# Optimization experiments

Measured on AMD Instinct MI355X. Metric: run time of the kernel, lower is better.

Reference implementation:

```python
import jax, jax.numpy as jnp
import numpy as np

EPS_F = 1e-6  # epsilon used when normalizing F^T F (as in EIGNN/MGNNI)


def _g(F):
    # g(F) = F^T F / (||F^T F||_F + eps): symmetric PSD, spectral radius <= 1
    FF = F.T @ F
    return FF / (jnp.linalg.norm(FF) + EPS_F)


def setup_inputs() -> dict:
    m, n = 128, 8192
    key = jax.random.key(0)
    k1, k2, k3, k4 = jax.random.split(key, 4)
    X = jax.random.normal(k1, (m, n), dtype=jnp.float32)
    # learned mixing matrix, init 1/sqrt(m) * randn as in __init__
    F = (1.0 / np.sqrt(m)) * jax.random.normal(k2, (m, m), dtype=jnp.float32)
    # precomputed eigendecomposition of the (normalized) adjacency S:
    # eigenvector matrix Q_S (n,n) and eigenvalues Lambda_S stored as (n,1)
    Q_S = jax.random.normal(k3, (n, n), dtype=jnp.float32) / np.sqrt(n)
    Lambda_S = (0.99 * (2.0 * jax.random.uniform(k4, (n, 1), dtype=jnp.float32) - 1.0))
    gamma = jnp.float32(0.8)
    return {"X": X, "F": F, "Q_S": Q_S, "Lambda_S": Lambda_S, "gamma": gamma}


def reference(X, F, Q_S, Lambda_S, gamma):
    # IDMFunction.forward: closed-form solve of Z = gamma * g(F) Z S + X
    # via eigendecompositions g(F) = Q_F diag(Lam_F) Q_F^T, S = Q_S diag(Lam_S) Q_S^T
    Lam_F, Q_F = jnp.linalg.eigh(_g(F))                         # (m,), (m,m)
    # G[i,j] = 1 / (1 - gamma * Lam_F[i] * Lam_S[j])            # (m,n)
    G = 1.0 / (1.0 - gamma * Lam_F[:, None] * Lambda_S.reshape(1, -1))
    # Z = Q_F (G * (Q_F^T X Q_S)) Q_S^T                          # (m,n)
    Z = Q_F @ (G * (Q_F.T @ X @ Q_S)) @ Q_S.T
    return Z
```

## Files before the change

### kernel.cpp

```cpp
#include <hip/hip_runtime.h>
#include <math.h>

#define EPS_F 1e-6f

typedef __attribute__((ext_vector_type(8))) short short8;
typedef __attribute__((ext_vector_type(4))) float f32x4;
typedef unsigned long long ull;

static __device__ __forceinline__ unsigned short f2bf(float f) {
    unsigned u = __float_as_uint(f);
    u += 0x7fff + ((u >> 16) & 1);
    return (unsigned short)(u >> 16);
}
static __device__ __forceinline__ ull pack4(float a, float b, float c, float d) {
    return (ull)f2bf(a) | ((ull)f2bf(b) << 16) | ((ull)f2bf(c) << 32) | ((ull)f2bf(d) << 48);
}
static __device__ __forceinline__ float bf2f(unsigned short s) {
    return __uint_as_float(((unsigned)s) << 16);
}


__global__ void kff(const float* __restrict__ F, float* __restrict__ FF) {
    int i = blockIdx.x, j = threadIdx.x;
    float s = 0.f;
    for (int k = 0; k < 128; ++k) s += F[k*128 + i] * F[k*128 + j];
    FF[i*128 + j] = s;
}

__global__ void knorm(const float* __restrict__ FF, float* __restrict__ inv) {
    float s = 0.f;
    for (int idx = threadIdx.x; idx < 128*128; idx += 256) { float v = FF[idx]; s += v*v; }
    for (int o = 32; o > 0; o >>= 1) s += __shfl_down(s, o);
    __shared__ float wsum[4];
    int lane = threadIdx.x & 63, w = threadIdx.x >> 6;
    if (lane == 0) wsum[w] = s;
    __syncthreads();
    if (threadIdx.x == 0) inv[0] = 1.f / (sqrtf(wsum[0]+wsum[1]+wsum[2]+wsum[3]) + EPS_F);
}

__global__ void kxbf(const float* __restrict__ X, short* __restrict__ Xb) {
    int i = blockIdx.x*blockDim.x + threadIdx.x;
    const float4* p = (const float4*)(X + (size_t)i*8);
    float4 v0 = p[0], v1 = p[1];
    *(ull*)&Xb[(size_t)i*8    ] = pack4(v0.x, v0.y, v0.z, v0.w);
    *(ull*)&Xb[(size_t)i*8 + 4] = pack4(v1.x, v1.y, v1.z, v1.w);
}

template<bool TRANSB>
__global__ __launch_bounds__(256) void gemm_p3(
    const short* __restrict__ Ab, const float* __restrict__ Qg,
    float* __restrict__ Cp, int N, int K, int KC)
{
    constexpr int LDT = 40;
    constexpr int ASZ = 128 * LDT;
    constexpr int BSZ = 64 * LDT;
    __shared__ short As[3 * ASZ];
    __shared__ short Bs[3 * BSZ];

    const int t    = threadIdx.x;
    const int lane = t & 63;
    const int w    = t >> 6;
    const int wm   = (w >> 1) * 64;
    const int wn   = (w & 1)  * 32;
    const int l16  = lane & 15;
    const int lq   = lane >> 4;
    const int n0   = blockIdx.x * 64;
    const int kb   = blockIdx.y * KC;
    const int NS   = KC >> 5;

    float* Cout = Cp + (size_t)blockIdx.y * (128 * 8192);

    const int ar0 = t >> 2, ako = (t & 3) * 8;
    const int br0 = t >> 3, bko = (t & 7) * 4;
    const int bn  = t & 63, bkh = t >> 6;

    f32x4 acc[4][2];
    #pragma unroll
    for (int i = 0; i < 4; ++i) { acc[i][0] = (f32x4){0,0,0,0}; acc[i][1] = (f32x4){0,0,0,0}; }

    short8 saA0, saA1, saB0, saB1;
    float4 sbA0, sbA1, sbB0, sbB1;
    float  sbtA[8], sbtB[8];

#define LOAD_T(k0, SA0, SA1, SB0, SB1, SBT) do {                                  \
        SA0 = *(const short8*)&Ab[(size_t)ar0*K + (k0) + ako];                    \
        SA1 = *(const short8*)&Ab[(size_t)(ar0+64)*K + (k0) + ako];               \
        if constexpr (TRANSB) {                                                   \
            SB0 = *(const float4*)&Qg[(size_t)(n0+br0   )*K + (k0) + bko];        \
            SB1 = *(const float4*)&Qg[(size_t)(n0+br0+32)*K + (k0) + bko];        \
        } else {                                                                  \
            _Pragma("unroll")                                                     \
            for (int j = 0; j < 8; ++j)                                           \
                SBT[j] = Qg[(size_t)((k0) + bkh*8 + j)*N + n0 + bn];              \
        }                                                                         \
    } while (0)

#define WRITE_T(buf, SA0, SA1, SB0, SB1, SBT) do {                                \
        short* asb = &As[(buf)*ASZ];                                              \
        short* bsb = &Bs[(buf)*BSZ];                                              \
        *(short8*)&asb[ar0*LDT + ako]      = SA0;                                 \
        *(short8*)&asb[(ar0+64)*LDT + ako] = SA1;                                 \
        if constexpr (TRANSB) {                                                   \
            *(ull*)&bsb[br0*LDT + bko]      = pack4(SB0.x, SB0.y, SB0.z, SB0.w);  \
            *(ull*)&bsb[(br0+32)*LDT + bko] = pack4(SB1.x, SB1.y, SB1.z, SB1.w);  \
        } else {                                                                  \
            short8 p;                                                             \
            _Pragma("unroll")                                                     \
            for (int j = 0; j < 8; ++j) p[j] = (short)f2bf(SBT[j]);               \
            *(short8*)&bsb[bn*LDT + bkh*8] = p;                                   \
        }                                                                         \
    } while (0)

#define MFMA_T(buf) do {                                                          \
        const short* asb = &As[(buf)*ASZ];                                        \
        const short* bsb = &Bs[(buf)*BSZ];                                        \
        short8 af[4], bfr[2];                                                     \
        _Pragma("unroll")                                                         \
        for (int mt = 0; mt < 4; ++mt)                                            \
            af[mt] = *(const short8*)&asb[(wm + mt*16 + l16)*LDT + lq*8];         \
        bfr[0] = *(const short8*)&bsb[(wn      + l16)*LDT + lq*8];                \
        bfr[1] = *(const short8*)&bsb[(wn + 16 + l16)*LDT + lq*8];                \
        _Pragma("unroll")                                                         \
        for (int mt = 0; mt < 4; ++mt) {                                          \
            acc[mt][0] = __builtin_amdgcn_mfma_f32_16x16x32_bf16(af[mt], bfr[0], acc[mt][0], 0, 0, 0); \
            acc[mt][1] = __builtin_amdgcn_mfma_f32_16x16x32_bf16(af[mt], bfr[1], acc[mt][1], 0, 0, 0); \
        }                                                                         \
    } while (0)

    LOAD_T(kb,      saA0, saA1, sbA0, sbA1, sbtA);
    LOAD_T(kb + 32, saB0, saB1, sbB0, sbB1, sbtB);
    WRITE_T(0, saA0, saA1, sbA0, sbA1, sbtA);
    __syncthreads();

    int b0 = 0, b1 = 1, b2 = 2;
    for (int ks = 0; ks < NS; ks += 2) {
        if (ks + 2 < NS) LOAD_T(kb + (ks+2)*32, saA0, saA1, sbA0, sbA1, sbtA);
        MFMA_T(b0);
        if (ks + 1 < NS) WRITE_T(b1, saB0, saB1, sbB0, sbB1, sbtB);
        __syncthreads();

        if (ks + 3 < NS) LOAD_T(kb + (ks+3)*32, saB0, saB1, sbB0, sbB1, sbtB);
        MFMA_T(b1);
        if (ks + 2 < NS) WRITE_T(b2, saA0, saA1, sbA0, sbA1, sbtA);
        __syncthreads();

        int tb = b0; b0 = b2; b2 = b1; b1 = tb;
    }

#undef LOAD_T
#undef WRITE_T
#undef MFMA_T

    #pragma unroll
    for (int mt = 0; mt < 4; ++mt)
        #pragma unroll
        for (int nt = 0; nt < 2; ++nt)
            #pragma unroll
            for (int r = 0; r < 4; ++r)
                Cout[(size_t)(wm + mt*16 + lq*4 + r)*N + n0 + wn + nt*16 + l16] = acc[mt][nt][r];
}

__global__ __launch_bounds__(512) void horner_fused(
    const float* __restrict__ FF, const float* __restrict__ invn,
    const float* __restrict__ lam, const float* __restrict__ gam,
    const float* __restrict__ Yp, short* __restrict__ Rg, int N)
{
    constexpr int LDT = 136;
    constexpr int T = 14;
    constexpr int SPL = 16;
    __shared__ short Abf[128 * LDT];
    __shared__ short Rs[32 * LDT];

    const int t    = threadIdx.x;
    const int lane = t & 63;
    const int w    = t >> 6;
    const int wm   = (w >> 1) * 32;
    const int wn   = (w & 1) * 16;
    const int l16  = lane & 15;
    const int lq   = lane >> 4;
    const int j0   = blockIdx.x * 32;

    #pragma unroll
    for (int i = 0; i < 8; ++i) {
        int flat = t + i*512;
        int m = flat >> 5, k4 = flat & 31;
        float4 v = *(const float4*)&FF[m*128 + k4*4];
        *(ull*)&Abf[m*LDT + k4*4] = pack4(v.x, v.y, v.z, v.w);
    }
    {
        int j = t & 31, mg = t >> 5;
        float vv[8];
        #pragma unroll
        for (int r2 = 0; r2 < 8; ++r2) {
            size_t idx = (size_t)(mg*8 + r2)*N + j0 + j;
            float s = 0.f;
            #pragma unroll
            for (int sp = 0; sp < SPL; ++sp) s += Yp[(size_t)sp*(128*8192) + idx];
            vv[r2] = s;
        }
        *(ull*)&Rs[j*LDT + mg*8    ] = pack4(vv[0], vv[1], vv[2], vv[3]);
        *(ull*)&Rs[j*LDT + mg*8 + 4] = pack4(vv[4], vv[5], vv[6], vv[7]);
    }
    __syncthreads();

    const int col = j0 + wn + l16;
    float yreg[2][4];
    #pragma unroll
    for (int mt = 0; mt < 2; ++mt)
        #pragma unroll
        for (int r = 0; r < 4; ++r)
            yreg[mt][r] = bf2f((unsigned short)Rs[(wn + l16)*LDT + wm + mt*16 + lq*4 + r]);
    const float s = gam[0] * lam[col] * invn[0];

    for (int it = 0; it < T; ++it) {
        f32x4 racc[2];
        racc[0] = (f32x4){0,0,0,0};
        racc[1] = (f32x4){0,0,0,0};
        #pragma unroll
        for (int kq = 0; kq < 4; ++kq) {
            short8 b  = *(const short8*)&Rs[(wn + l16)*LDT + kq*32 + lq*8];
            short8 a0 = *(const short8*)&Abf[(wm      + l16)*LDT + kq*32 + lq*8];
            short8 a1 = *(const short8*)&Abf[(wm + 16 + l16)*LDT + kq*32 + lq*8];
            racc[0] = __builtin_amdgcn_mfma_f32_16x16x32_bf16(a0, b, racc[0], 0, 0, 0);
            racc[1] = __builtin_amdgcn_mfma_f32_16x16x32_bf16(a1, b, racc[1], 0, 0, 0);
        }
        __syncthreads();
        #pragma unroll
        for (int mt = 0; mt < 2; ++mt) {
            float r0 = yreg[mt][0] + s*racc[mt][0];
            float r1 = yreg[mt][1] + s*racc[mt][1];
            float r2 = yreg[mt][2] + s*racc[mt][2];
            float r3 = yreg[mt][3] + s*racc[mt][3];
            if (it < T-1) {
                *(ull*)&Rs[(wn + l16)*LDT + wm + mt*16 + lq*4] = pack4(r0, r1, r2, r3);
            } else {
                int row = wm + mt*16 + lq*4;
                Rg[(size_t)(row+0)*N + col] = (short)f2bf(r0);
                Rg[(size_t)(row+1)*N + col] = (short)f2bf(r1);
                Rg[(size_t)(row+2)*N + col] = (short)f2bf(r2);
                Rg[(size_t)(row+3)*N + col] = (short)f2bf(r3);
            }
        }
        if (it < T-1) __syncthreads();
    }
}

__global__ __launch_bounds__(256) void zred(const float* __restrict__ Zp,
                                            float* __restrict__ Z) {
    int i = (blockIdx.x*blockDim.x + threadIdx.x) * 4;
    f32x4 s = (f32x4){0,0,0,0};
    #pragma unroll
    for (int sp = 0; sp < 8; ++sp) {
        const float4 v = *(const float4*)&Zp[(size_t)sp*(128*8192) + i];
        s[0] += v.x; s[1] += v.y; s[2] += v.z; s[3] += v.w;
    }
    *(f32x4*)&Z[i] = s;
}


extern "C" void kernel_launch(void* const* d_in, const int* in_sizes, int n_in,
                              void* d_out, int out_size, void* d_ws, size_t ws_size,
                              hipStream_t stream) {
    const float* X   = (const float*)d_in[0];
    const float* F   = (const float*)d_in[1];
    const float* Q   = (const float*)d_in[2];
    const float* lam = (const float*)d_in[3];
    const float* gam = (const float*)d_in[4];
    float* Z = (float*)d_out;

    const int N = 8192, K = 8192;

    char* ws = (char*)d_ws;
    float* FF  = (float*)(ws);
    float* inv = (float*)(ws + 65536);
    short* Xb  = (short*)(ws + 131072);
    short* Rg  = (short*)(ws + 2228224);
    float* Yp  = (float*)(ws + 4325376);
    float* Zp  = (float*)(ws + 4325376 + 67108864);

    hipLaunchKernelGGL(kff,   dim3(128), dim3(128), 0, stream, F, FF);
    hipLaunchKernelGGL(knorm, dim3(1),   dim3(256), 0, stream, FF, inv);
    hipLaunchKernelGGL(kxbf,  dim3(512), dim3(256), 0, stream, X, Xb);

    hipLaunchKernelGGL((gemm_p3<false>), dim3(128, 16), dim3(256), 0, stream,
                       Xb, Q, Yp, N, K, 512);

    hipLaunchKernelGGL(horner_fused, dim3(256), dim3(512), 0, stream,
                       FF, inv, lam, gam, Yp, Rg, N);

    hipLaunchKernelGGL((gemm_p3<true>), dim3(128, 8), dim3(256), 0, stream,
                       Rg, Q, Zp, N, K, 1024);

    hipLaunchKernelGGL(zred, dim3(1024), dim3(256), 0, stream, Zp, Z);
}
```

Before: 219.1 us.

## Halve split-K for first GEMM and switch to double-buffered LDS with lighter barriers

The first GEMM's split-K factor drops from 16 to 8 (KC 512 to 1024), and horner_fused now reduces 8 partial slices instead of 16. This halves the fp32 partial-sum traffic that goes to and from the Yp workspace. Both GEMMs move from triple-buffered to double-buffered shared memory, and __syncthreads is replaced by a barrier that waits only on LDS counters, which cuts LDS use and may raise occupancy. The cost is fewer blocks in the first GEMM, so parallelism is lower, and there is less slack between global loads and their use.

```diff
diff --git a/kernel.cpp b/kernel.cpp
--- a/kernel.cpp
+++ b/kernel.cpp
@@ -18,6 +18,12 @@
 static __device__ __forceinline__ float bf2f(unsigned short s) {
     return __uint_as_float(((unsigned)s) << 16);
 }
+
+#define BAR() do {                                            \
+        asm volatile("s_waitcnt lgkmcnt(0)" ::: "memory");    \
+        __builtin_amdgcn_s_barrier();                         \
+        __builtin_amdgcn_sched_barrier(0);                    \
+    } while (0)
 
 
 __global__ void kff(const float* __restrict__ F, float* __restrict__ FF) {
@@ -47,15 +53,15 @@
 }
 
 template<bool TRANSB>
-__global__ __launch_bounds__(256) void gemm_p3(
+__global__ __launch_bounds__(256) void gemm_pipe(
     const short* __restrict__ Ab, const float* __restrict__ Qg,
     float* __restrict__ Cp, int N, int K, int KC)
 {
     constexpr int LDT = 40;
     constexpr int ASZ = 128 * LDT;
     constexpr int BSZ = 64 * LDT;
-    __shared__ short As[3 * ASZ];
-    __shared__ short Bs[3 * BSZ];
+    __shared__ short As[2][ASZ];
+    __shared__ short Bs[2][BSZ];
 
     const int t    = threadIdx.x;
     const int lane = t & 63;
@@ -96,30 +102,26 @@
     } while (0)
 
 #define WRITE_T(buf, SA0, SA1, SB0, SB1, SBT) do {                                \
-        short* asb = &As[(buf)*ASZ];                                              \
-        short* bsb = &Bs[(buf)*BSZ];                                              \
-        *(short8*)&asb[ar0*LDT + ako]      = SA0;                                 \
-        *(short8*)&asb[(ar0+64)*LDT + ako] = SA1;                                 \
+        *(short8*)&As[buf][ar0*LDT + ako]      = SA0;                             \
+        *(short8*)&As[buf][(ar0+64)*LDT + ako] = SA1;                             \
         if constexpr (TRANSB) {                                                   \
-            *(ull*)&bsb[br0*LDT + bko]      = pack4(SB0.x, SB0.y, SB0.z, SB0.w);  \
-            *(ull*)&bsb[(br0+32)*LDT + bko] = pack4(SB1.x, SB1.y, SB1.z, SB1.w);  \
+            *(ull*)&Bs[buf][br0*LDT + bko]      = pack4(SB0.x, SB0.y, SB0.z, SB0.w); \
+            *(ull*)&Bs[buf][(br0+32)*LDT + bko] = pack4(SB1.x, SB1.y, SB1.z, SB1.w); \
         } else {                                                                  \
             short8 p;                                                             \
             _Pragma("unroll")                                                     \
             for (int j = 0; j < 8; ++j) p[j] = (short)f2bf(SBT[j]);               \
-            *(short8*)&bsb[bn*LDT + bkh*8] = p;                                   \
+            *(short8*)&Bs[buf][bn*LDT + bkh*8] = p;                               \
         }                                                                         \
     } while (0)
 
 #define MFMA_T(buf) do {                                                          \
-        const short* asb = &As[(buf)*ASZ];                                        \
-        const short* bsb = &Bs[(buf)*BSZ];                                        \
         short8 af[4], bfr[2];                                                     \
         _Pragma("unroll")                                                         \
         for (int mt = 0; mt < 4; ++mt)                                            \
-            af[mt] = *(const short8*)&asb[(wm + mt*16 + l16)*LDT + lq*8];         \
-        bfr[0] = *(const short8*)&bsb[(wn      + l16)*LDT + lq*8];                \
-        bfr[1] = *(const short8*)&bsb[(wn + 16 + l16)*LDT + lq*8];                \
+            af[mt] = *(const short8*)&As[buf][(wm + mt*16 + l16)*LDT + lq*8];     \
+        bfr[0] = *(const short8*)&Bs[buf][(wn      + l16)*LDT + lq*8];            \
+        bfr[1] = *(const short8*)&Bs[buf][(wn + 16 + l16)*LDT + lq*8];            \
         _Pragma("unroll")                                                         \
         for (int mt = 0; mt < 4; ++mt) {                                          \
             acc[mt][0] = __builtin_amdgcn_mfma_f32_16x16x32_bf16(af[mt], bfr[0], acc[mt][0], 0, 0, 0); \
@@ -130,21 +132,18 @@
     LOAD_T(kb,      saA0, saA1, sbA0, sbA1, sbtA);
     LOAD_T(kb + 32, saB0, saB1, sbB0, sbB1, sbtB);
     WRITE_T(0, saA0, saA1, sbA0, sbA1, sbtA);
-    __syncthreads();
-
-    int b0 = 0, b1 = 1, b2 = 2;
+    BAR();
+
     for (int ks = 0; ks < NS; ks += 2) {
         if (ks + 2 < NS) LOAD_T(kb + (ks+2)*32, saA0, saA1, sbA0, sbA1, sbtA);
-        MFMA_T(b0);
-        if (ks + 1 < NS) WRITE_T(b1, saB0, saB1, sbB0, sbB1, sbtB);
-        __syncthreads();
+        MFMA_T(0);
+        if (ks + 1 < NS) WRITE_T(1, saB0, saB1, sbB0, sbB1, sbtB);
+        BAR();
 
         if (ks + 3 < NS) LOAD_T(kb + (ks+3)*32, saB0, saB1, sbB0, sbB1, sbtB);
-        MFMA_T(b1);
-        if (ks + 2 < NS) WRITE_T(b2, saA0, saA1, sbA0, sbA1, sbtA);
-        __syncthreads();
-
-        int tb = b0; b0 = b2; b2 = b1; b1 = tb;
+        MFMA_T(1);
+        if (ks + 2 < NS) WRITE_T(0, saA0, saA1, sbA0, sbA1, sbtA);
+        BAR();
     }
 
 #undef LOAD_T
@@ -167,7 +166,7 @@
 {
     constexpr int LDT = 136;
     constexpr int T = 14;
-    constexpr int SPL = 16;
+    constexpr int SPL = 8;
     __shared__ short Abf[128 * LDT];
     __shared__ short Rs[32 * LDT];
 
@@ -276,19 +275,19 @@
     short* Xb  = (short*)(ws + 131072);
     short* Rg  = (short*)(ws + 2228224);
     float* Yp  = (float*)(ws + 4325376);
-    float* Zp  = (float*)(ws + 4325376 + 67108864);
+    float* Zp  = (float*)(ws + 4325376 + 33554432);
 
     hipLaunchKernelGGL(kff,   dim3(128), dim3(128), 0, stream, F, FF);
     hipLaunchKernelGGL(knorm, dim3(1),   dim3(256), 0, stream, FF, inv);
     hipLaunchKernelGGL(kxbf,  dim3(512), dim3(256), 0, stream, X, Xb);
 
-    hipLaunchKernelGGL((gemm_p3<false>), dim3(128, 16), dim3(256), 0, stream,
-                       Xb, Q, Yp, N, K, 512);
+    hipLaunchKernelGGL((gemm_pipe<false>), dim3(128, 8), dim3(256), 0, stream,
+                       Xb, Q, Yp, N, K, 1024);
 
     hipLaunchKernelGGL(horner_fused, dim3(256), dim3(512), 0, stream,
                        FF, inv, lam, gam, Yp, Rg, N);
 
-    hipLaunchKernelGGL((gemm_p3<true>), dim3(128, 8), dim3(256), 0, stream,
+    hipLaunchKernelGGL((gemm_pipe<true>), dim3(128, 8), dim3(256), 0, stream,
                        Rg, Q, Zp, N, K, 1024);
 
     hipLaunchKernelGGL(zred, dim3(1024), dim3(256), 0, stream, Zp, Z);
```

Result: faster. 205.8 us (-6.1%).
